# Kernel optimization log

Hardware: AMD Instinct MI355X
Metric: run time of the kernel (lower is better)

Reference implementation:

```python
import jax, jax.numpy as jnp
import numpy as np

B, L, F_, T = 64, 49, 2048, 32
V, E, H, A = 15000, 512, 512, 512

def _w(key, shape, scale=0.02):
    return (scale * jax.random.normal(key, shape)).astype(jnp.float32)

def setup_inputs() -> dict:
    key = jax.random.key(0)
    ks = jax.random.split(key, 24)
    inp = {
        "features": jax.random.normal(ks[0], (B, L, F_), dtype=jnp.float32),
        "captions": jax.random.randint(ks[1], (B, T), 0, V),
        "force_prob": 1,
        # parameters (torch nn.Linear convention: W [out,in])
        "init_h_W": _w(ks[2], (H, F_)), "init_h_b": jnp.zeros((H,), jnp.float32),
        "init_c_W": _w(ks[3], (H, F_)), "init_c_b": jnp.zeros((H,), jnp.float32),
        "W_a_W": _w(ks[4], (A, F_)), "W_a_b": jnp.zeros((A,), jnp.float32),
        "U_a_W": _w(ks[5], (A, H)), "U_a_b": jnp.zeros((A,), jnp.float32),
        "v_a_W": _w(ks[6], (1, A)), "v_a_b": jnp.zeros((1,), jnp.float32),
        "embed_table": _w(ks[7], (V, E), 1.0),
        "lstm_W_ih": _w(ks[8], (4 * H, E + F_)), "lstm_W_hh": _w(ks[9], (4 * H, H)),
        "lstm_b_ih": jnp.zeros((4 * H,), jnp.float32), "lstm_b_hh": jnp.zeros((4 * H,), jnp.float32),
        "fc_W": _w(ks[10], (V, H)), "fc_b": jnp.zeros((V,), jnp.float32),
    }
    return inp

def _decoder(features, captions,
             init_h_W, init_h_b, init_c_W, init_c_b,
             W_a_W, W_a_b, U_a_W, U_a_b, v_a_W, v_a_b,
             embed_table, lstm_W_ih, lstm_W_hh, lstm_b_ih, lstm_b_hh,
             fc_W, fc_b):
    emb = embed_table[captions]                      # [B,T,E]
    mean_f = jnp.mean(features, axis=1)              # [B,F]
    h0 = mean_f @ init_h_W.T + init_h_b              # [B,H]
    c0 = mean_f @ init_c_W.T + init_c_b
    # features are constant over time -> precompute W_a(features) once
    att1 = jnp.einsum('blf,af->bla', features, W_a_W) + W_a_b  # [B,L,A]

    def step(carry, w_emb):
        h, c = carry
        att2 = h @ U_a_W.T + U_a_b                   # [B,A]
        score = jnp.tanh(att1 + att2[:, None, :]) @ v_a_W[0] + v_a_b[0]  # [B,L]
        w = jax.nn.softmax(score, axis=1)            # [B,L]
        context = jnp.einsum('bl,blf->bf', w, features)  # [B,F]
        x = jnp.concatenate([w_emb, context], axis=1)     # [B,E+F]
        gates = x @ lstm_W_ih.T + lstm_b_ih + h @ lstm_W_hh.T + lstm_b_hh
        i, f, g, o = jnp.split(gates, 4, axis=1)
        i, f, o = jax.nn.sigmoid(i), jax.nn.sigmoid(f), jax.nn.sigmoid(o)
        g = jnp.tanh(g)
        c_new = f * c + i * g
        h_new = o * jnp.tanh(c_new)                  # dropout p=0 (eval) = identity
        logits = h_new @ fc_W.T + fc_b               # [B,V]
        return (h_new, c_new), logits

    _, logits = jax.lax.scan(step, (h0, c0), jnp.swapaxes(emb, 0, 1))  # [T,B,V]
    return jnp.transpose(logits, (1, 0, 2))          # [B,T,V]

def reference(features, captions, force_prob,
              init_h_W, init_h_b, init_c_W, init_c_b,
              W_a_W, W_a_b, U_a_W, U_a_b, v_a_W, v_a_b,
              embed_table, lstm_W_ih, lstm_W_hh, lstm_b_ih, lstm_b_hh,
              fc_W, fc_b):
    # force_prob == 1 -> teacher forcing at every step (sampling branch never taken)
    return _decoder(features, captions,
                    init_h_W, init_h_b, init_c_W, init_c_b,
                    W_a_W, W_a_b, U_a_W, U_a_b, v_a_W, v_a_b,
                    embed_table, lstm_W_ih, lstm_W_hh, lstm_b_ih, lstm_b_hh,
                    fc_W, fc_b)
```

## Files before the change

### kernel.cpp

```cpp
#include <hip/hip_runtime.h>
#include <math.h>

#define B_ 64
#define L_ 49
#define F_DIM 2048
#define T_ 32
#define V_ 15000
#define E_ 512
#define H_ 512
#define A_ 512

typedef __attribute__((ext_vector_type(8))) short s16x8;
typedef __attribute__((ext_vector_type(4))) short s16x4;
typedef __attribute__((ext_vector_type(4))) float f32x4;

__device__ __forceinline__ unsigned short f2b(float x) {
    union { float f; unsigned int u; } v; v.f = x;
    unsigned int r = v.u + 0x7FFF + ((v.u >> 16) & 1);
    return (unsigned short)(r >> 16);
}
__device__ __forceinline__ float b2f(unsigned short u) {
    union { unsigned int i; float f; } v; v.i = ((unsigned int)u) << 16; return v.f;
}
__device__ __forceinline__ float rcp_fast(float x) {
    return __builtin_amdgcn_rcpf(x);
}
__device__ __forceinline__ float tanhf_fast(float x) {
    x = fminf(fmaxf(x, -15.f), 15.f);
    const float e = __expf(2.f * x);
    return (e - 1.f) * rcp_fast(e + 1.f);
}
__device__ __forceinline__ float sigmoid_fast(float x) {
    return rcp_fast(1.f + __expf(-x));
}

__device__ __forceinline__ float aload_f(const float* p) {
    return __hip_atomic_load((const float*)p, __ATOMIC_RELAXED, __HIP_MEMORY_SCOPE_AGENT);
}
__device__ __forceinline__ void astore_f(float* p, float v) {
    __hip_atomic_store(p, v, __ATOMIC_RELAXED, __HIP_MEMORY_SCOPE_AGENT);
}
__device__ __forceinline__ unsigned long long aload_u64(const void* p) {
    return __hip_atomic_load((const unsigned long long*)p, __ATOMIC_RELAXED, __HIP_MEMORY_SCOPE_AGENT);
}
__device__ __forceinline__ void astore_u32(void* p, unsigned v) {
    __hip_atomic_store((unsigned*)p, v, __ATOMIC_RELAXED, __HIP_MEMORY_SCOPE_AGENT);
}
__device__ __forceinline__ unsigned apoll(const unsigned* p) {
    return __hip_atomic_load(p, __ATOMIC_RELAXED, __HIP_MEMORY_SCOPE_AGENT);
}
__device__ __forceinline__ void aset(unsigned* p, unsigned v) {
    __hip_atomic_store(p, v, __ATOMIC_RELAXED, __HIP_MEMORY_SCOPE_AGENT);
}

__global__ __launch_bounds__(256)
void k_castall(const float* __restrict__ feat, const float* __restrict__ W_a,
               const float* __restrict__ W_ih, const float* __restrict__ fc_W,
               unsigned short* __restrict__ feat_bf,
               unsigned short* __restrict__ wcomb_bf,
               unsigned short* __restrict__ fcW_bf)
{
    const int r  = blockIdx.y;
    const int c4 = blockIdx.x * 256 + threadIdx.x;
    const float* src;
    unsigned short* dst;
    int cols;
    if (r < 3136)      { src = feat + (size_t)r * 2048;                 dst = feat_bf + (size_t)r * 2048;            cols = 2048; }
    else if (r < 3648) { const int rr = r - 3136; src = W_a + (size_t)rr * 2048;              dst = wcomb_bf + (size_t)rr * 2048;          cols = 2048; }
    else if (r < 5696) { const int rr = r - 3648; src = W_ih + (size_t)rr * 2560 + 512;       dst = wcomb_bf + (size_t)(rr + 512) * 2048;  cols = 2048; }
    else               { const int rr = r - 5696; src = fc_W + (size_t)rr * 512;              dst = fcW_bf + (size_t)rr * 512;             cols = 512; }
    if (c4 * 4 >= cols) return;
    float4 v = *reinterpret_cast<const float4*>(src + c4 * 4);
    ushort4 o;
    o.x = f2b(v.x); o.y = f2b(v.y); o.z = f2b(v.z); o.w = f2b(v.w);
    *reinterpret_cast<ushort4*>(dst + c4 * 4) = o;
}

#define LDSW 40
__global__ __launch_bounds__(256)
void gemm_mfma(const unsigned short* __restrict__ A, int lda,
               const void* __restrict__ W0p, int ldw0, int N0,
               const void* __restrict__ W1p, int ldw1, int w32,
               const float* __restrict__ bias0, const float* __restrict__ bias1,
               float* __restrict__ C, int ldc,
               int M, int N, int K, int permT, int obf)
{
    __shared__ unsigned short As[128 * LDSW];
    __shared__ unsigned short Ws[128 * LDSW];

    const int tid  = threadIdx.x;
    const int m0   = blockIdx.x * 128;
    const int n0   = blockIdx.y * 128;
    const int wave = tid >> 6;
    const int lane = tid & 63;
    const int wr   = (wave >> 1) * 64;
    const int wc   = (wave & 1) * 64;

    f32x4 acc[4][4];
    #pragma unroll
    for (int i = 0; i < 4; ++i)
        #pragma unroll
        for (int j = 0; j < 4; ++j)
            acc[i][j] = (f32x4)(0.f);

    const int fr = lane & 15;
    const int fk = (lane >> 4) * 8;

    for (int kc = 0; kc < K; kc += 32) {
        ushort4 av[2][2], wv[2][2];
        #pragma unroll
        for (int i = 0; i < 2; ++i) {
            const int idx = tid + i * 256;
            const int row = idx >> 2;
            const int seg = idx & 3;
            av[i][0] = make_ushort4(0, 0, 0, 0); av[i][1] = make_ushort4(0, 0, 0, 0);
            wv[i][0] = make_ushort4(0, 0, 0, 0); wv[i][1] = make_ushort4(0, 0, 0, 0);
            if (m0 + row < M) {
                const float4 t0 = *reinterpret_cast<const float4*>(
                    A + (size_t)(m0 + row) * lda + kc + seg * 8);
                *reinterpret_cast<float4*>(&av[i][0]) = t0;
            }
            const int n_abs = n0 + row;
            if (n_abs < N) {
                if (w32) {
                    const float* wrow = (n_abs < N0)
                        ? ((const float*)W0p + (size_t)n_abs * ldw0)
                        : ((const float*)W1p + (size_t)(n_abs - N0) * ldw1);
                    const float4 x = *reinterpret_cast<const float4*>(wrow + kc + seg * 8);
                    const float4 y = *reinterpret_cast<const float4*>(wrow + kc + seg * 8 + 4);
                    wv[i][0] = make_ushort4(f2b(x.x), f2b(x.y), f2b(x.z), f2b(x.w));
                    wv[i][1] = make_ushort4(f2b(y.x), f2b(y.y), f2b(y.z), f2b(y.w));
                } else {
                    const unsigned short* wrow = (n_abs < N0)
                        ? ((const unsigned short*)W0p + (size_t)n_abs * ldw0)
                        : ((const unsigned short*)W1p + (size_t)(n_abs - N0) * ldw1);
                    const float4 t0 = *reinterpret_cast<const float4*>(wrow + kc + seg * 8);
                    *reinterpret_cast<float4*>(&wv[i][0]) = t0;
                }
            }
        }
        __syncthreads();
        #pragma unroll
        for (int i = 0; i < 2; ++i) {
            const int idx = tid + i * 256;
            const int row = idx >> 2;
            const int seg = idx & 3;
            *reinterpret_cast<ushort4*>(&As[row * LDSW + seg * 8])     = av[i][0];
            *reinterpret_cast<ushort4*>(&As[row * LDSW + seg * 8 + 4]) = av[i][1];
            *reinterpret_cast<ushort4*>(&Ws[row * LDSW + seg * 8])     = wv[i][0];
            *reinterpret_cast<ushort4*>(&Ws[row * LDSW + seg * 8 + 4]) = wv[i][1];
        }
        __syncthreads();

        s16x8 afr[4], bfr[4];
        #pragma unroll
        for (int mf = 0; mf < 4; ++mf)
            afr[mf] = *reinterpret_cast<const s16x8*>(&As[(wr + mf * 16 + fr) * LDSW + fk]);
        #pragma unroll
        for (int nf = 0; nf < 4; ++nf)
            bfr[nf] = *reinterpret_cast<const s16x8*>(&Ws[(wc + nf * 16 + fr) * LDSW + fk]);

        #pragma unroll
        for (int mf = 0; mf < 4; ++mf)
            #pragma unroll
            for (int nf = 0; nf < 4; ++nf)
                acc[mf][nf] = __builtin_amdgcn_mfma_f32_16x16x32_bf16(
                    afr[mf], bfr[nf], acc[mf][nf], 0, 0, 0);
    }

    const int cr = (lane >> 4) * 4;
    const int cc = lane & 15;
    #pragma unroll
    for (int nf = 0; nf < 4; ++nf) {
        const int n = n0 + wc + nf * 16 + cc;
        if (n >= N) continue;
        float bv = 0.f;
        if (bias0 && n < N0) bv += bias0[n];
        if (bias1) bv += bias1[n];
        #pragma unroll
        for (int mf = 0; mf < 4; ++mf) {
            #pragma unroll
            for (int r = 0; r < 4; ++r) {
                const int m = m0 + wr + mf * 16 + cr + r;
                if (m >= M) continue;
                const size_t row = permT ? ((size_t)(m & 63) * permT + (size_t)(m >> 6))
                                         : (size_t)m;
                const float v = acc[mf][nf][r] + bv;
                if (obf) ((unsigned short*)C)[row * (size_t)ldc + n] = f2b(v);
                else     C[row * (size_t)ldc + n] = v;
            }
        }
    }
}

__global__ __launch_bounds__(256)
void gemm64(const float* __restrict__ A, int lda,
            const float* __restrict__ W0, int ldw0, int N0,
            const float* __restrict__ W1, int ldw1,
            const float* __restrict__ bias0, const float* __restrict__ bias1,
            float* __restrict__ C, int ldc,
            int N, int K, int obf, float* __restrict__ C2)
{
    __shared__ float As[16][64];
    __shared__ float Ws[16][64];

    const int tid = threadIdx.x;
    const int m0  = blockIdx.x * 64;
    const int n0  = blockIdx.y * 64;

    const int lr = tid >> 2;
    const int kq = tid & 3;

    const int n_abs = n0 + lr;
    const bool wvalid = (n_abs < N);
    const float* wrow = nullptr;
    if (wvalid)
        wrow = (n_abs < N0) ? (W0 + (size_t)n_abs * ldw0)
                            : (W1 + (size_t)(n_abs - N0) * ldw1);
    const float* arow = A + (size_t)(m0 + lr) * lda;

    const int ty = tid >> 4;
    const int tx = tid & 15;

    float acc[4][4] = {{0.f}};

    for (int kc = 0; kc < K; kc += 16) {
        float4 av = *reinterpret_cast<const float4*>(arow + kc + kq * 4);
        float4 wv = make_float4(0.f, 0.f, 0.f, 0.f);
        if (wvalid)
            wv = *reinterpret_cast<const float4*>(wrow + kc + kq * 4);

        __syncthreads();
        As[kq * 4 + 0][lr] = av.x;
        As[kq * 4 + 1][lr] = av.y;
        As[kq * 4 + 2][lr] = av.z;
        As[kq * 4 + 3][lr] = av.w;
        Ws[kq * 4 + 0][lr] = wv.x;
        Ws[kq * 4 + 1][lr] = wv.y;
        Ws[kq * 4 + 2][lr] = wv.z;
        Ws[kq * 4 + 3][lr] = wv.w;
        __syncthreads();

        #pragma unroll
        for (int kk = 0; kk < 16; ++kk) {
            const float4 a4 = *reinterpret_cast<const float4*>(&As[kk][ty * 4]);
            const float4 w4 = *reinterpret_cast<const float4*>(&Ws[kk][tx * 4]);
            const float aa[4] = {a4.x, a4.y, a4.z, a4.w};
            const float ww[4] = {w4.x, w4.y, w4.z, w4.w};
            #pragma unroll
            for (int i = 0; i < 4; ++i)
                #pragma unroll
                for (int j = 0; j < 4; ++j)
                    acc[i][j] = fmaf(aa[i], ww[j], acc[i][j]);
        }
    }

    #pragma unroll
    for (int i = 0; i < 4; ++i) {
        const int m = m0 + ty * 4 + i;
        #pragma unroll
        for (int j = 0; j < 4; ++j) {
            const int n = n0 + tx * 4 + j;
            if (n >= N) continue;
            float v = acc[i][j];
            if (bias0 && n < N0) v += bias0[n];
            if (bias1 && n >= N0) v += bias1[n - N0];
            if (obf == 2) {
                if (n < N0) ((unsigned short*)C)[(size_t)m * N0 + n] = f2b(v);
                else        C2[(size_t)m * (N - N0) + (n - N0)] = v;
            } else if (obf == 1) {
                ((unsigned short*)C)[(size_t)m * ldc + n] = f2b(v);
            } else {
                C[(size_t)m * ldc + n] = v;
            }
        }
    }
}

__global__ __launch_bounds__(256)
void k_mean(const float* __restrict__ feat, float* __restrict__ mean_f)
{
    const int idx = blockIdx.x * 256 + threadIdx.x;
    const int b = idx >> 11;
    const int f = idx & 2047;
    const float* p = feat + (size_t)b * L_ * F_DIM + f;
    float s = 0.f;
    #pragma unroll 7
    for (int l = 0; l < L_; ++l) s += p[(size_t)l * F_DIM];
    mean_f[idx] = s * (1.0f / 49.0f);
}

__global__ __launch_bounds__(256)
void k_embgather(const float* __restrict__ table, const int* __restrict__ caps,
                 unsigned short* __restrict__ emb_bf)
{
    const int idx = blockIdx.x * 256 + threadIdx.x;
    const int e   = idx & 511;
    const int row = idx >> 9;
    const int t   = row >> 6;
    const int b   = row & 63;
    const int tok = caps[b * T_ + t];
    emb_bf[idx] = f2b(table[(size_t)tok * E_ + e]);
}

#define NBLK_RECUR 80u

__global__ __launch_bounds__(512)
void k_recur(unsigned short* __restrict__ hbf,
             float* __restrict__ att2g,
             const float* __restrict__ U_a,
             const float* __restrict__ W_hh,
             const float* __restrict__ U_a_b,
             const unsigned short* __restrict__ attFb,
             const float* __restrict__ g_emb,
             const float* __restrict__ v_w, const float* __restrict__ v_b,
             const float* __restrict__ c0,
             unsigned short* __restrict__ h_hist,
             unsigned* __restrict__ bar)
{
    const int g   = blockIdx.x;
    const int tid = threadIdx.x;

    __shared__ unsigned short Wc[32 * 520];
    __shared__ unsigned short hsd[64 * 520];
    __shared__ float a2[512];
    __shared__ float wl[64];
    __shared__ float gates[2048];
    __shared__ float hs[512];
    __shared__ float vws[512];
    __shared__ float vub[512];

    const int R    = g * 32;
    const int wave = tid >> 6;
    const int lane = tid & 63;

    for (int idx = tid; idx < 4096; idx += 512) {
        const int r  = idx >> 7;
        const int kq = idx & 127;
        const int n  = R + r;
        const float* src = (n < 512) ? (U_a + (size_t)n * 512)
                                     : (W_hh + (size_t)(n - 512) * 512);
        float4 v = *reinterpret_cast<const float4*>(src + kq * 4);
        unsigned short* d = &Wc[r * 520 + kq * 4];
        d[0] = f2b(v.x); d[1] = f2b(v.y); d[2] = f2b(v.z); d[3] = f2b(v.w);
    }
    vws[tid] = v_w[tid];
    vub[tid] = U_a_b[tid];

    const int isB = (g < 64);
    const int b   = g;
    const float vb0 = v_b[0];

    const int ggrp = tid >> 7;
    const int jj   = (tid & 127) * 4;
    const int gc   = ggrp * 512 + jj;
    float creg = 0.f;
    if (isB) creg = c0[b * 512 + tid];

    const int tcol  = wave >> 2;
    const int rows0 = (wave & 3) * 16;
    const int frow  = lane & 15;
    const int fko   = (lane >> 4) * 8;
    __syncthreads();

    for (int t = 0; t < T_; ++t) {
        if (t > 0) {
            if (tid < 64) {
                while (!__all((int)(apoll(bar + tid * 16) >= (unsigned)t)))
                    __builtin_amdgcn_s_sleep(1);
            }
            __syncthreads();
        }

        {
            unsigned long long v[16];
            #pragma unroll
            for (int k = 0; k < 16; ++k)
                v[k] = aload_u64((const unsigned char*)hbf + ((size_t)(tid + k * 512)) * 8);
            #pragma unroll
            for (int k = 0; k < 16; ++k) {
                const int s   = tid + k * 512;
                const int row = s >> 7;
                const int c   = s & 127;
                *reinterpret_cast<unsigned long long*>(&hsd[row * 520 + c * 4]) = v[k];
            }
        }
        __syncthreads();

        {
            f32x4 acc = (f32x4)(0.f);
            #pragma unroll
            for (int ks = 0; ks < 16; ++ks) {
                const s16x8 af = *reinterpret_cast<const s16x8*>(
                    &hsd[(rows0 + frow) * 520 + ks * 32 + fko]);
                const s16x8 bf = *reinterpret_cast<const s16x8*>(
                    &Wc[(tcol * 16 + frow) * 520 + ks * 32 + fko]);
                acc = __builtin_amdgcn_mfma_f32_16x16x32_bf16(af, bf, acc, 0, 0, 0);
            }
            const int col = R + tcol * 16 + frow;
            #pragma unroll
            for (int r = 0; r < 4; ++r) {
                const int babs = rows0 + (lane >> 4) * 4 + r;
                astore_f(&att2g[(size_t)babs * 2560 + col], acc[r]);
            }
        }
        asm volatile("s_waitcnt vmcnt(0)" ::: "memory");
        __syncthreads();
        if (tid == 0) {
            if (g < 16) aset(bar + 1024 + g * 16, (unsigned)(t + 1));
            aset(bar + 1280 + g * 16, (unsigned)(t + 1));
        }

        if (isB) {
            s16x8 a1pf[7];
            #pragma unroll
            for (int i = 0; i < 7; ++i) {
                int l = wave + i * 8; if (l > 48) l = 48;
                a1pf[i] = *reinterpret_cast<const s16x8*>(
                    attFb + (size_t)(b * L_ + l) * 2560 + lane * 8);
            }
            const float4 ge = *reinterpret_cast<const float4*>(
                g_emb + ((size_t)t * 64 + b) * 2048 + gc);

            if (tid < 64) {
                while (!__all((int)(tid >= 16 ||
                        apoll(bar + 1024 + tid * 16) >= (unsigned)(t + 1))))
                    __builtin_amdgcn_s_sleep(1);
            }
            __syncthreads();

            a2[tid] = aload_f(&att2g[(size_t)b * 2560 + tid]) + vub[tid];
            __syncthreads();

            #pragma unroll
            for (int i = 0; i < 7; ++i) {
                const int l = wave + i * 8;
                if (l < L_) {
                    float s = 0.f;
                    #pragma unroll
                    for (int j = 0; j < 8; ++j)
                        s += tanhf_fast(b2f((unsigned short)a1pf[i][j]) + a2[lane * 8 + j]) * vws[lane * 8 + j];
                    #pragma unroll
                    for (int off = 32; off > 0; off >>= 1) s += __shfl_down(s, off);
                    if (lane == 0) wl[l] = s + vb0;
                }
            }
            __syncthreads();

            if (tid < 64) {
                float v = (tid < L_) ? wl[tid] : -3.0e38f;
                float mx = v;
                #pragma unroll
                for (int off = 32; off > 0; off >>= 1) mx = fmaxf(mx, __shfl_xor(mx, off));
                float e = (tid < L_) ? __expf(v - mx) : 0.f;
                float sum = e;
                #pragma unroll
                for (int off = 32; off > 0; off >>= 1) sum += __shfl_xor(sum, off);
                if (tid < L_) wl[tid] = e * rcp_fast(sum);
            }

            if (tid < 64) {
                for (;;) {
                    const unsigned v0 = apoll(bar + 1280 + tid * 16);
                    const unsigned v1 = (tid < 16) ? apoll(bar + 1280 + (tid + 64) * 16)
                                                   : 0xFFFFFFFFu;
                    if (__all((int)(v0 >= (unsigned)(t + 1) && v1 >= (unsigned)(t + 1)))) break;
                    __builtin_amdgcn_s_sleep(1);
                }
            }
            __syncthreads();

            {
                union { unsigned long long u; float f[2]; } q0, q1;
                q0.u = aload_u64(&att2g[(size_t)b * 2560 + 512 + gc]);
                q1.u = aload_u64(&att2g[(size_t)b * 2560 + 512 + gc + 2]);
                float s0 = ge.x + q0.f[0];
                float s1 = ge.y + q0.f[1];
                float s2 = ge.z + q1.f[0];
                float s3 = ge.w + q1.f[1];
                const unsigned short* fp = attFb + (size_t)(b * L_) * 2560 + 512 + gc;
                #pragma unroll 7
                for (int l = 0; l < L_; ++l) {
                    const float w = wl[l];
                    const s16x4 v = *reinterpret_cast<const s16x4*>(fp + (size_t)l * 2560);
                    s0 = fmaf(w, b2f((unsigned short)v[0]), s0);
                    s1 = fmaf(w, b2f((unsigned short)v[1]), s1);
                    s2 = fmaf(w, b2f((unsigned short)v[2]), s2);
                    s3 = fmaf(w, b2f((unsigned short)v[3]), s3);
                }
                *reinterpret_cast<float4*>(&gates[gc]) = make_float4(s0, s1, s2, s3);
            }
            __syncthreads();

            {
                const float gi = gates[tid],        gf = gates[512 + tid];
                const float gg = gates[1024 + tid], go = gates[1536 + tid];
                const float i = sigmoid_fast(gi);
                const float f = sigmoid_fast(gf);
                const float gv = tanhf_fast(gg);
                const float o = sigmoid_fast(go);
                creg = f * creg + i * gv;
                hs[tid] = o * tanhf_fast(creg);
            }
            __syncthreads();

            if (tid < 256) {
                const unsigned lo = f2b(hs[2 * tid]);
                const unsigned hi = f2b(hs[2 * tid + 1]);
                const unsigned pk = lo | (hi << 16);
                astore_u32((unsigned*)hbf + b * 256 + tid, pk);
                ((unsigned*)h_hist)[(size_t)(t * 64 + b) * 256 + tid] = pk;
            }
            asm volatile("s_waitcnt vmcnt(0)" ::: "memory");
            __syncthreads();
            if (tid == 0) aset(bar + b * 16, (unsigned)(t + 1));
        }
    }
}

extern "C" void kernel_launch(void* const* d_in, const int* in_sizes, int n_in,
                              void* d_out, int out_size, void* d_ws, size_t ws_size,
                              hipStream_t stream)
{
    const float* features = (const float*)d_in[0];
    const int*   captions = (const int*)d_in[1];
    const float* init_h_W = (const float*)d_in[3];
    const float* init_h_b = (const float*)d_in[4];
    const float* init_c_W = (const float*)d_in[5];
    const float* init_c_b = (const float*)d_in[6];
    const float* W_a_W    = (const float*)d_in[7];
    const float* W_a_b    = (const float*)d_in[8];
    const float* U_a_W    = (const float*)d_in[9];
    const float* U_a_b    = (const float*)d_in[10];
    const float* v_a_W    = (const float*)d_in[11];
    const float* v_a_b    = (const float*)d_in[12];
    const float* embed    = (const float*)d_in[13];
    const float* W_ih     = (const float*)d_in[14];
    const float* W_hh     = (const float*)d_in[15];
    const float* b_ih     = (const float*)d_in[16];
    const float* b_hh     = (const float*)d_in[17];
    const float* fc_W     = (const float*)d_in[18];
    const float* fc_b     = (const float*)d_in[19];
    float* out = (float*)d_out;

    float* ws      = (float*)d_ws;
    float* mean_f  = ws;
    float* c_st    = ws + 131072;
    unsigned short* h_bf   = (unsigned short*)(ws + 163840);
    unsigned short* h_hist = (unsigned short*)(ws + 180224);
    float* att2g   = ws + 704512;
    unsigned short* fcW_bf = (unsigned short*)(ws + 868352);
    unsigned* bar  = (unsigned*)(ws + 4708352);

    float* g_emb = out;
    unsigned short* attF_bf  = (unsigned short*)(out + 4194304);
    unsigned short* feat_bf  = (unsigned short*)(out + 13000000);
    unsigned short* wcomb_bf = (unsigned short*)(out + 17000000);
    unsigned short* emb_bf   = (unsigned short*)(out + 20000000);

    k_mean<<<512, 256, 0, stream>>>(features, mean_f);

    gemm64<<<dim3(1, 16), 256, 0, stream>>>(mean_f, F_DIM,
                                            init_h_W, F_DIM, H_,
                                            init_c_W, F_DIM,
                                            init_h_b, init_c_b,
                                            (float*)h_bf, H_, 2 * H_, F_DIM,
                                            2, c_st);

    k_embgather<<<4096, 256, 0, stream>>>(embed, captions, emb_bf);
    gemm_mfma<<<dim3(16, 16), 256, 0, stream>>>(emb_bf, E_,
                                                W_ih, E_ + F_DIM, 4 * H_,
                                                nullptr, 0, 1,
                                                b_ih, b_hh,
                                                g_emb, 4 * H_,
                                                2048, 4 * H_, E_, 0, 0);

    k_castall<<<dim3(2, 20696), 256, 0, stream>>>(features, W_a_W, W_ih, fc_W,
                                                  feat_bf, wcomb_bf, fcW_bf);

    gemm_mfma<<<dim3(25, 20), 256, 0, stream>>>(feat_bf, F_DIM,
                                                wcomb_bf, 2048, 512,
                                                wcomb_bf + (size_t)512 * 2048, 2048, 0,
                                                W_a_b, nullptr,
                                                (float*)attF_bf, 2560,
                                                3136, 2560, F_DIM, 0, 1);

    hipMemsetAsync(bar, 0, 12288, stream);
    k_recur<<<NBLK_RECUR, 512, 0, stream>>>(h_bf, att2g, U_a_W, W_hh, U_a_b,
                                            attF_bf, g_emb, v_a_W, v_a_b,
                                            c_st, h_hist, bar);

    gemm_mfma<<<dim3(16, 118), 256, 0, stream>>>(h_hist, H_,
                                                 fcW_bf, H_, V_,
                                                 nullptr, 0, 0,
                                                 fc_b, nullptr,
                                                 out, V_, 2048, V_, H_, 32, 0);
}
```

Before: 719.2 us.

## Compute attention projection locally per batch block to cut a grid barrier per step

The attention projection h@U_a^T is now computed redundantly in each of the 64 batch blocks from a pre-transposed bf16 copy of U_a, built by a new transpose-cast kernel. This removes the 16 blocks that previously produced att2 through global memory and one cross-block wait per timestep. The persistent grid shrinks from 80 to 64 blocks, each owning W_hh columns. Attention scoring and softmax now run before the h-exchange barrier. The cost is extra per-block scalar FMA work over 512x512 per step and a larger MFMA share per block.

```diff
diff --git a/kernel.cpp b/kernel.cpp
--- a/kernel.cpp
+++ b/kernel.cpp
@@ -74,6 +74,27 @@
     ushort4 o;
     o.x = f2b(v.x); o.y = f2b(v.y); o.z = f2b(v.z); o.w = f2b(v.w);
     *reinterpret_cast<ushort4*>(dst + c4 * 4) = o;
+}
+
+__global__ __launch_bounds__(256)
+void k_castT(const float* __restrict__ U, unsigned short* __restrict__ UT)
+{
+    __shared__ float tile[64][65];
+    const int a0 = blockIdx.x * 64;
+    const int k0 = blockIdx.y * 64;
+    const int c  = threadIdx.x & 63;
+    const int r0 = threadIdx.x >> 6;
+    #pragma unroll
+    for (int rr = 0; rr < 16; ++rr) {
+        const int r = r0 * 16 + rr;
+        tile[r][c] = U[(size_t)(a0 + r) * 512 + k0 + c];
+    }
+    __syncthreads();
+    #pragma unroll
+    for (int rr = 0; rr < 16; ++rr) {
+        const int r = r0 * 16 + rr;
+        UT[(size_t)(k0 + r) * 512 + a0 + c] = f2b(tile[c][r]);
+    }
 }
 
 #define LDSW 40
@@ -303,12 +324,12 @@
     emb_bf[idx] = f2b(table[(size_t)tok * E_ + e]);
 }
 
-#define NBLK_RECUR 80u
+#define NBLK_RECUR 64u
 
 __global__ __launch_bounds__(512)
 void k_recur(unsigned short* __restrict__ hbf,
              float* __restrict__ att2g,
-             const float* __restrict__ U_a,
+             const unsigned short* __restrict__ uaT,
              const float* __restrict__ W_hh,
              const float* __restrict__ U_a_b,
              const unsigned short* __restrict__ attFb,
@@ -319,10 +340,12 @@
              unsigned* __restrict__ bar)
 {
     const int g   = blockIdx.x;
+    const int b   = g;
     const int tid = threadIdx.x;
 
     __shared__ unsigned short Wc[32 * 520];
     __shared__ unsigned short hsd[64 * 520];
+    __shared__ float red[4][512];
     __shared__ float a2[512];
     __shared__ float wl[64];
     __shared__ float gates[2048];
@@ -330,32 +353,29 @@
     __shared__ float vws[512];
     __shared__ float vub[512];
 
-    const int R    = g * 32;
     const int wave = tid >> 6;
     const int lane = tid & 63;
 
     for (int idx = tid; idx < 4096; idx += 512) {
         const int r  = idx >> 7;
         const int kq = idx & 127;
-        const int n  = R + r;
-        const float* src = (n < 512) ? (U_a + (size_t)n * 512)
-                                     : (W_hh + (size_t)(n - 512) * 512);
+        const float* src = W_hh + (size_t)(g * 32 + r) * 512;
         float4 v = *reinterpret_cast<const float4*>(src + kq * 4);
         unsigned short* d = &Wc[r * 520 + kq * 4];
         d[0] = f2b(v.x); d[1] = f2b(v.y); d[2] = f2b(v.z); d[3] = f2b(v.w);
     }
     vws[tid] = v_w[tid];
     vub[tid] = U_a_b[tid];
-
-    const int isB = (g < 64);
-    const int b   = g;
+    hs[tid]  = b2f(hbf[b * 512 + tid]);
     const float vb0 = v_b[0];
 
     const int ggrp = tid >> 7;
     const int jj   = (tid & 127) * 4;
     const int gc   = ggrp * 512 + jj;
-    float creg = 0.f;
-    if (isB) creg = c0[b * 512 + tid];
+    float creg = c0[b * 512 + tid];
+
+    const int aq = tid & 127;
+    const int kc = tid >> 7;
 
     const int tcol  = wave >> 2;
     const int rows0 = (wave & 3) * 16;
@@ -363,14 +383,72 @@
     const int fko   = (lane >> 4) * 8;
     __syncthreads();
 
+    s16x8 a1pf[7];
+    #pragma unroll
+    for (int i = 0; i < 7; ++i) {
+        int l = wave + i * 8; if (l > 48) l = 48;
+        a1pf[i] = *reinterpret_cast<const s16x8*>(
+            attFb + (size_t)(b * L_ + l) * 2560 + lane * 8);
+    }
+
     for (int t = 0; t < T_; ++t) {
+        {
+            float p0 = 0.f, p1 = 0.f, p2 = 0.f, p3 = 0.f;
+            const unsigned short* up = uaT + ((size_t)kc * 128) * 512 + aq * 4;
+            #pragma unroll 4
+            for (int k = 0; k < 128; ++k) {
+                const float hk = hs[kc * 128 + k];
+                const s16x4 u = *reinterpret_cast<const s16x4*>(up + (size_t)k * 512);
+                p0 = fmaf(hk, b2f((unsigned short)u[0]), p0);
+                p1 = fmaf(hk, b2f((unsigned short)u[1]), p1);
+                p2 = fmaf(hk, b2f((unsigned short)u[2]), p2);
+                p3 = fmaf(hk, b2f((unsigned short)u[3]), p3);
+            }
+            red[kc][aq * 4 + 0] = p0;
+            red[kc][aq * 4 + 1] = p1;
+            red[kc][aq * 4 + 2] = p2;
+            red[kc][aq * 4 + 3] = p3;
+        }
+        __syncthreads();
+        a2[tid] = red[0][tid] + red[1][tid] + red[2][tid] + red[3][tid] + vub[tid];
+        __syncthreads();
+
+        #pragma unroll
+        for (int i = 0; i < 7; ++i) {
+            const int l = wave + i * 8;
+            if (l < L_) {
+                float s = 0.f;
+                #pragma unroll
+                for (int j = 0; j < 8; ++j)
+                    s += tanhf_fast(b2f((unsigned short)a1pf[i][j]) + a2[lane * 8 + j]) * vws[lane * 8 + j];
+                #pragma unroll
+                for (int off = 32; off > 0; off >>= 1) s += __shfl_down(s, off);
+                if (lane == 0) wl[l] = s + vb0;
+            }
+        }
+        __syncthreads();
+
+        if (tid < 64) {
+            float v = (tid < L_) ? wl[tid] : -3.0e38f;
+            float mx = v;
+            #pragma unroll
+            for (int off = 32; off > 0; off >>= 1) mx = fmaxf(mx, __shfl_xor(mx, off));
+            float e = (tid < L_) ? __expf(v - mx) : 0.f;
+            float sum = e;
+            #pragma unroll
+            for (int off = 32; off > 0; off >>= 1) sum += __shfl_xor(sum, off);
+            if (tid < L_) wl[tid] = e * rcp_fast(sum);
+        }
+        const float4 ge = *reinterpret_cast<const float4*>(
+            g_emb + ((size_t)t * 64 + b) * 2048 + gc);
+
         if (t > 0) {
             if (tid < 64) {
                 while (!__all((int)(apoll(bar + tid * 16) >= (unsigned)t)))
                     __builtin_amdgcn_s_sleep(1);
             }
-            __syncthreads();
-        }
+        }
+        __syncthreads();
 
         {
             unsigned long long v[16];
@@ -397,124 +475,67 @@
                     &Wc[(tcol * 16 + frow) * 520 + ks * 32 + fko]);
                 acc = __builtin_amdgcn_mfma_f32_16x16x32_bf16(af, bf, acc, 0, 0, 0);
             }
-            const int col = R + tcol * 16 + frow;
+            const int col = g * 32 + tcol * 16 + frow;
             #pragma unroll
             for (int r = 0; r < 4; ++r) {
                 const int babs = rows0 + (lane >> 4) * 4 + r;
-                astore_f(&att2g[(size_t)babs * 2560 + col], acc[r]);
+                astore_f(&att2g[(size_t)babs * 2048 + col], acc[r]);
             }
         }
         asm volatile("s_waitcnt vmcnt(0)" ::: "memory");
         __syncthreads();
-        if (tid == 0) {
-            if (g < 16) aset(bar + 1024 + g * 16, (unsigned)(t + 1));
-            aset(bar + 1280 + g * 16, (unsigned)(t + 1));
-        }
-
-        if (isB) {
-            s16x8 a1pf[7];
-            #pragma unroll
-            for (int i = 0; i < 7; ++i) {
-                int l = wave + i * 8; if (l > 48) l = 48;
-                a1pf[i] = *reinterpret_cast<const s16x8*>(
-                    attFb + (size_t)(b * L_ + l) * 2560 + lane * 8);
-            }
-            const float4 ge = *reinterpret_cast<const float4*>(
-                g_emb + ((size_t)t * 64 + b) * 2048 + gc);
-
-            if (tid < 64) {
-                while (!__all((int)(tid >= 16 ||
-                        apoll(bar + 1024 + tid * 16) >= (unsigned)(t + 1))))
-                    __builtin_amdgcn_s_sleep(1);
-            }
-            __syncthreads();
-
-            a2[tid] = aload_f(&att2g[(size_t)b * 2560 + tid]) + vub[tid];
-            __syncthreads();
-
-            #pragma unroll
-            for (int i = 0; i < 7; ++i) {
-                const int l = wave + i * 8;
-                if (l < L_) {
-                    float s = 0.f;
-                    #pragma unroll
-                    for (int j = 0; j < 8; ++j)
-                        s += tanhf_fast(b2f((unsigned short)a1pf[i][j]) + a2[lane * 8 + j]) * vws[lane * 8 + j];
-                    #pragma unroll
-                    for (int off = 32; off > 0; off >>= 1) s += __shfl_down(s, off);
-                    if (lane == 0) wl[l] = s + vb0;
-                }
-            }
-            __syncthreads();
-
-            if (tid < 64) {
-                float v = (tid < L_) ? wl[tid] : -3.0e38f;
-                float mx = v;
-                #pragma unroll
-                for (int off = 32; off > 0; off >>= 1) mx = fmaxf(mx, __shfl_xor(mx, off));
-                float e = (tid < L_) ? __expf(v - mx) : 0.f;
-                float sum = e;
-                #pragma unroll
-                for (int off = 32; off > 0; off >>= 1) sum += __shfl_xor(sum, off);
-                if (tid < L_) wl[tid] = e * rcp_fast(sum);
-            }
-
-            if (tid < 64) {
-                for (;;) {
-                    const unsigned v0 = apoll(bar + 1280 + tid * 16);
-                    const unsigned v1 = (tid < 16) ? apoll(bar + 1280 + (tid + 64) * 16)
-                                                   : 0xFFFFFFFFu;
-                    if (__all((int)(v0 >= (unsigned)(t + 1) && v1 >= (unsigned)(t + 1)))) break;
-                    __builtin_amdgcn_s_sleep(1);
-                }
-            }
-            __syncthreads();
-
-            {
-                union { unsigned long long u; float f[2]; } q0, q1;
-                q0.u = aload_u64(&att2g[(size_t)b * 2560 + 512 + gc]);
-                q1.u = aload_u64(&att2g[(size_t)b * 2560 + 512 + gc + 2]);
-                float s0 = ge.x + q0.f[0];
-                float s1 = ge.y + q0.f[1];
-                float s2 = ge.z + q1.f[0];
-                float s3 = ge.w + q1.f[1];
-                const unsigned short* fp = attFb + (size_t)(b * L_) * 2560 + 512 + gc;
-                #pragma unroll 7
-                for (int l = 0; l < L_; ++l) {
-                    const float w = wl[l];
-                    const s16x4 v = *reinterpret_cast<const s16x4*>(fp + (size_t)l * 2560);
-                    s0 = fmaf(w, b2f((unsigned short)v[0]), s0);
-                    s1 = fmaf(w, b2f((unsigned short)v[1]), s1);
-                    s2 = fmaf(w, b2f((unsigned short)v[2]), s2);
-                    s3 = fmaf(w, b2f((unsigned short)v[3]), s3);
-                }
-                *reinterpret_cast<float4*>(&gates[gc]) = make_float4(s0, s1, s2, s3);
-            }
-            __syncthreads();
-
-            {
-                const float gi = gates[tid],        gf = gates[512 + tid];
-                const float gg = gates[1024 + tid], go = gates[1536 + tid];
-                const float i = sigmoid_fast(gi);
-                const float f = sigmoid_fast(gf);
-                const float gv = tanhf_fast(gg);
-                const float o = sigmoid_fast(go);
-                creg = f * creg + i * gv;
-                hs[tid] = o * tanhf_fast(creg);
-            }
-            __syncthreads();
-
-            if (tid < 256) {
-                const unsigned lo = f2b(hs[2 * tid]);
-                const unsigned hi = f2b(hs[2 * tid + 1]);
-                const unsigned pk = lo | (hi << 16);
-                astore_u32((unsigned*)hbf + b * 256 + tid, pk);
-                ((unsigned*)h_hist)[(size_t)(t * 64 + b) * 256 + tid] = pk;
-            }
-            asm volatile("s_waitcnt vmcnt(0)" ::: "memory");
-            __syncthreads();
-            if (tid == 0) aset(bar + b * 16, (unsigned)(t + 1));
-        }
+        if (tid == 0) aset(bar + 1024 + g * 16, (unsigned)(t + 1));
+
+        if (tid < 64) {
+            while (!__all((int)(apoll(bar + 1024 + tid * 16) >= (unsigned)(t + 1))))
+                __builtin_amdgcn_s_sleep(1);
+        }
+        __syncthreads();
+
+        {
+            union { unsigned long long u; float f[2]; } q0, q1;
+            q0.u = aload_u64(&att2g[(size_t)b * 2048 + gc]);
+            q1.u = aload_u64(&att2g[(size_t)b * 2048 + gc + 2]);
+            float s0 = ge.x + q0.f[0];
+            float s1 = ge.y + q0.f[1];
+            float s2 = ge.z + q1.f[0];
+            float s3 = ge.w + q1.f[1];
+            const unsigned short* fp = attFb + (size_t)(b * L_) * 2560 + 512 + gc;
+            #pragma unroll 7
+            for (int l = 0; l < L_; ++l) {
+                const float w = wl[l];
+                const s16x4 v = *reinterpret_cast<const s16x4*>(fp + (size_t)l * 2560);
+                s0 = fmaf(w, b2f((unsigned short)v[0]), s0);
+                s1 = fmaf(w, b2f((unsigned short)v[1]), s1);
+                s2 = fmaf(w, b2f((unsigned short)v[2]), s2);
+                s3 = fmaf(w, b2f((unsigned short)v[3]), s3);
+            }
+            *reinterpret_cast<float4*>(&gates[gc]) = make_float4(s0, s1, s2, s3);
+        }
+        __syncthreads();
+
+        {
+            const float gi = gates[tid],        gf = gates[512 + tid];
+            const float gg = gates[1024 + tid], go = gates[1536 + tid];
+            const float i = sigmoid_fast(gi);
+            const float f = sigmoid_fast(gf);
+            const float gv = tanhf_fast(gg);
+            const float o = sigmoid_fast(go);
+            creg = f * creg + i * gv;
+            hs[tid] = o * tanhf_fast(creg);
+        }
+        __syncthreads();
+
+        if (tid < 256) {
+            const unsigned lo = f2b(hs[2 * tid]);
+            const unsigned hi = f2b(hs[2 * tid + 1]);
+            const unsigned pk = lo | (hi << 16);
+            astore_u32((unsigned*)hbf + b * 256 + tid, pk);
+            ((unsigned*)h_hist)[(size_t)(t * 64 + b) * 256 + tid] = pk;
+        }
+        asm volatile("s_waitcnt vmcnt(0)" ::: "memory");
+        __syncthreads();
+        if (tid == 0) aset(bar + b * 16, (unsigned)(t + 1));
     }
 }
 
@@ -551,6 +572,7 @@
     float* att2g   = ws + 704512;
     unsigned short* fcW_bf = (unsigned short*)(ws + 868352);
     unsigned* bar  = (unsigned*)(ws + 4708352);
+    unsigned short* uaT_bf = (unsigned short*)(ws + 4720000);
 
     float* g_emb = out;
     unsigned short* attF_bf  = (unsigned short*)(out + 4194304);
@@ -577,6 +599,7 @@
 
     k_castall<<<dim3(2, 20696), 256, 0, stream>>>(features, W_a_W, W_ih, fc_W,
                                                   feat_bf, wcomb_bf, fcW_bf);
+    k_castT<<<dim3(8, 8), 256, 0, stream>>>(U_a_W, uaT_bf);
 
     gemm_mfma<<<dim3(25, 20), 256, 0, stream>>>(feat_bf, F_DIM,
                                                 wcomb_bf, 2048, 512,
@@ -586,7 +609,7 @@
                                                 3136, 2560, F_DIM, 0, 1);
 
     hipMemsetAsync(bar, 0, 12288, stream);
-    k_recur<<<NBLK_RECUR, 512, 0, stream>>>(h_bf, att2g, U_a_W, W_hh, U_a_b,
+    k_recur<<<NBLK_RECUR, 512, 0, stream>>>(h_bf, att2g, uaT_bf, W_hh, U_a_b,
                                             attF_bf, g_emb, v_a_W, v_a_b,
                                             c_st, h_hist, bar);
 
```

Measured after the change: 940.1 us. 30.7% more time.
